# Kernel optimization log

Measured on AMD Instinct MI355X. Metric: run time of the kernel, lower is better.

Reference implementation:

```python
import jax, jax.numpy as jnp
import numpy as np

N = 50000      # nodes
E = 800000     # edges (avg degree 16)
EMB = 128      # emb_dim
NF = 7         # x_features
EF = 5         # edge_features
L = 5          # num_layer
BN_EPS = 1e-5


def setup_inputs() -> dict:
    key = jax.random.key(0)
    ks = jax.random.split(key, 12)
    s = 0.05
    return {
        "x": jax.random.normal(ks[0], (N, NF), jnp.float32),
        "edge_attr": jax.random.normal(ks[1], (E, EF), jnp.float32),
        "edge_index": jax.random.randint(ks[2], (2, E), 0, N, dtype=jnp.int32),
        "W_x": jax.random.normal(ks[3], (NF, EMB), jnp.float32) * s,
        "b_x": jax.random.normal(ks[4], (NF, EMB), jnp.float32) * s,
        "W_e": jax.random.normal(ks[5], (L, EF, EMB), jnp.float32) * s,
        "b_e": jax.random.normal(ks[6], (L, EF, EMB), jnp.float32) * s,
        # per-layer GIN update MLP: Linear(EMB,2EMB)-ReLU-Linear(2EMB,EMB)
        "W1": jax.random.normal(ks[7], (L, EMB, 2 * EMB), jnp.float32) * s,
        "b1": jnp.zeros((L, 2 * EMB), jnp.float32),
        "W2": jax.random.normal(ks[8], (L, 2 * EMB, EMB), jnp.float32) * s,
        "b2": jnp.zeros((L, EMB), jnp.float32),
        # per-layer BatchNorm1d affine params
        "gamma": jnp.ones((L, EMB), jnp.float32),
        "beta": jnp.zeros((L, EMB), jnp.float32),
    }


def reference(x, edge_attr, W_x, b_x, W_e, b_e, W1, b1, W2, b2, gamma, beta, edge_index):
    src, dst = edge_index[0], edge_index[1]
    # initial node embedding: sum of 7 Linear(1,EMB) applied per column == x @ W_x + sum(biases)
    h = x @ W_x + b_x.sum(axis=0)  # [N, EMB]
    for l in range(L):
        # edge embeddings: sum of EF Linear(1,EMB) over edge_attr columns
        e_emb = edge_attr @ W_e[l] + b_e[l].sum(axis=0)  # [E, EMB]
        sl_emb = b_e[l].sum(axis=0)  # self-loop edges have zero attr -> bias sum
        # message = x_j + edge_emb, aggr = add (scatter over dst); self loops add h + sl_emb
        msg = h[src] + e_emb                                        # [E, EMB]
        agg = jax.ops.segment_sum(msg, dst, num_segments=N) + h + sl_emb  # [N, EMB]
        # GIN update MLP
        z = jax.nn.relu(agg @ W1[l] + b1[l]) @ W2[l] + b2[l]        # [N, EMB]
        # BatchNorm1d (training-mode batch stats, biased variance)
        mu = z.mean(axis=0)
        var = z.var(axis=0)
        z = (z - mu) * jax.lax.rsqrt(var + BN_EPS) * gamma[l] + beta[l]
        # ELU on all but last layer; dropout is identity at drop_ratio=0; JK='last'
        h = jax.nn.elu(z) if l < L - 1 else z
    return h
```

## Files before the change

kernel.cpp:

```cpp
#include <hip/hip_runtime.h>
#include <math.h>

#define NN 50000
#define NE 800000
#define EMB 128
#define HID 256
#define NF 7
#define EF 5
#define NL 5
#define BN_EPS 1e-5f
#define NREP 32
#define SCAN_B 196

typedef _Float16 f16x8 __attribute__((ext_vector_type(8)));
typedef _Float16 f16x2 __attribute__((ext_vector_type(2)));
typedef __attribute__((ext_vector_type(4))) float f32x4;

__device__ inline unsigned pkh2(float a, float b) {
    union { unsigned v; _Float16 h[2]; } x;
    x.h[0] = (_Float16)a; x.h[1] = (_Float16)b;
    return x.v;
}
__device__ inline float2 uph2(unsigned u) {
    union { unsigned v; _Float16 h[2]; } x; x.v = u;
    return make_float2((float)x.h[0], (float)x.h[1]);
}
__device__ inline unsigned short f2h_bits(float f) {
    _Float16 h = (_Float16)f;
    return __builtin_bit_cast(unsigned short, h);
}
__device__ inline float h_bits2f(unsigned short b) {
    return (float)__builtin_bit_cast(_Float16, b);
}
__device__ inline f16x2 as_h2(unsigned u) { return __builtin_bit_cast(f16x2, u); }

__global__ void k_prep(const float* __restrict__ b_x, const float* __restrict__ b_e,
                       float* __restrict__ bsum_x, float* __restrict__ bsum_e,
                       int* __restrict__ counts, int* __restrict__ cursor) {
    int tid = threadIdx.x;
    if (blockIdx.x == 0 && tid < EMB) {
        float s = 0.f;
        for (int f = 0; f < NF; ++f) s += b_x[f * EMB + tid];
        bsum_x[tid] = s;
        for (int l = 0; l < NL; ++l) {
            float se = 0.f;
            for (int f = 0; f < EF; ++f) se += b_e[(l * EF + f) * EMB + tid];
            bsum_e[l * EMB + tid] = se;
        }
    }
    int gid = blockIdx.x * blockDim.x + tid;
    int stride = gridDim.x * blockDim.x;
    for (int i = gid; i < NN; i += stride) { counts[i] = 0; cursor[i] = 0; }
}

__global__ void k_prepw(const float* __restrict__ W1, const float* __restrict__ W2,
                        unsigned short* __restrict__ W1ph, unsigned short* __restrict__ W1pl,
                        unsigned short* __restrict__ W2ph, unsigned short* __restrict__ W2pl) {
    const int TOT = NL * EMB * HID;
    int gid = blockIdx.x * blockDim.x + threadIdx.x;
    if (gid < TOT) {
        int l = gid / (EMB * HID);
        int r = gid % (EMB * HID);
        int w = r >> 13;
        int rem = r & 8191;
        int h2 = rem >> 11;
        int rem2 = rem & 2047;
        int kk = rem2 >> 9;
        int rem3 = rem2 & 511;
        int lane = rem3 >> 3;
        int j = rem3 & 7;
        int hc = w * 64 + h2 * 16 + (lane & 15);
        int k = kk * 32 + (lane >> 4) * 8 + j;
        float wv = W1[((size_t)l * EMB + k) * HID + hc];
        unsigned short hi = f2h_bits(wv);
        W1ph[gid] = hi;
        W1pl[gid] = f2h_bits(wv - h_bits2f(hi));
    } else if (gid < 2 * TOT) {
        int g = gid - TOT;
        int l = g / (EMB * HID);
        int r = g % (EMB * HID);
        int w = r >> 13;
        int rem = r & 8191;
        int o2 = rem >> 12;
        int rem2 = rem & 4095;
        int kk = rem2 >> 9;
        int rem3 = rem2 & 511;
        int lane = rem3 >> 3;
        int j = rem3 & 7;
        int oc = w * 32 + o2 * 16 + (lane & 15);
        int k2 = kk * 32 + (lane >> 4) * 8 + j;
        float wv = W2[((size_t)l * HID + k2) * EMB + oc];
        unsigned short hi = f2h_bits(wv);
        W2ph[g] = hi;
        W2pl[g] = f2h_bits(wv - h_bits2f(hi));
    }
}

__global__ void k_init(const float* __restrict__ x, const float* __restrict__ W_x,
                       const float* __restrict__ bsum_x, unsigned short* __restrict__ h16) {
    int gid = blockIdx.x * blockDim.x + threadIdx.x;
    int v = gid >> 5;
    if (v >= NN) return;
    int c = (gid & 31) << 2;
    float4 acc = *(const float4*)(bsum_x + c);
    #pragma unroll
    for (int f = 0; f < NF; ++f) {
        float xv = x[(size_t)v * NF + f];
        float4 w = *(const float4*)(W_x + f * EMB + c);
        acc.x += xv * w.x; acc.y += xv * w.y; acc.z += xv * w.z; acc.w += xv * w.w;
    }
    uint2 p = make_uint2(pkh2(acc.x, acc.y), pkh2(acc.z, acc.w));
    *(uint2*)(h16 + (size_t)v * EMB + c) = p;
}

__global__ void k_hist(const int* __restrict__ dst, int* __restrict__ counts) {
    int e = blockIdx.x * blockDim.x + threadIdx.x;
    if (e < NE) atomicAdd(&counts[dst[e]], 1);
}

__global__ void k_scan1(const int* __restrict__ counts, int* __restrict__ bsum) {
    int tid = threadIdx.x;
    int i = blockIdx.x * 256 + tid;
    int v = (i < NN) ? counts[i] : 0;
    #pragma unroll
    for (int off = 1; off < 64; off <<= 1) v += __shfl_xor(v, off, 64);
    __shared__ int ws[4];
    if ((tid & 63) == 0) ws[tid >> 6] = v;
    __syncthreads();
    if (tid == 0) bsum[blockIdx.x] = ws[0] + ws[1] + ws[2] + ws[3];
}

__global__ void k_scan2(const int* __restrict__ bsum, int* __restrict__ bpre,
                        int* __restrict__ row_start) {
    int tid = threadIdx.x;
    int x = (tid < SCAN_B) ? bsum[tid] : 0;
    int lane = tid & 63, wv = tid >> 6;
    int v = x;
    #pragma unroll
    for (int off = 1; off < 64; off <<= 1) {
        int t = __shfl_up(v, off, 64);
        if (lane >= off) v += t;
    }
    __shared__ int wsum[4];
    if (lane == 63) wsum[wv] = v;
    __syncthreads();
    int woff = 0;
    #pragma unroll
    for (int w = 0; w < 4; ++w) if (w < wv) woff += wsum[w];
    int incl = v + woff;
    if (tid < SCAN_B) bpre[tid] = incl - x;
    if (tid == 255) row_start[NN] = incl;
}

__global__ void k_scan3(const int* __restrict__ counts, const int* __restrict__ bpre,
                        int* __restrict__ row_start) {
    int tid = threadIdx.x;
    int i = blockIdx.x * 256 + tid;
    int x = (i < NN) ? counts[i] : 0;
    int lane = tid & 63, wv = tid >> 6;
    int v = x;
    #pragma unroll
    for (int off = 1; off < 64; off <<= 1) {
        int t = __shfl_up(v, off, 64);
        if (lane >= off) v += t;
    }
    __shared__ int wsum[4];
    if (lane == 63) wsum[wv] = v;
    __syncthreads();
    int woff = 0;
    #pragma unroll
    for (int w = 0; w < 4; ++w) if (w < wv) woff += wsum[w];
    if (i < NN) row_start[i] = bpre[blockIdx.x] + v + woff - x;
}

__global__ void k_fill(const int* __restrict__ src, const int* __restrict__ dst,
                       const float* __restrict__ edge_attr,
                       const int* __restrict__ row_start, int* __restrict__ cursor,
                       uint4* __restrict__ sorted_pk) {
    int e = blockIdx.x * blockDim.x + threadIdx.x;
    if (e >= NE) return;
    int d = dst[e];
    int pos = atomicAdd(&cursor[d], 1);
    int idx = row_start[d] + pos;
    const float* ea = edge_attr + (size_t)e * EF;
    float a0 = ea[0], a1 = ea[1], a2 = ea[2], a3 = ea[3], a4 = ea[4];
    uint4 pk;
    pk.x = (unsigned)src[e];
    pk.y = pkh2(a0, a1);
    pk.z = pkh2(a2, a3);
    pk.w = pkh2(a4, 0.f);
    sorted_pk[idx] = pk;
}

__global__ void k_esum(const uint4* __restrict__ sorted_pk,
                       const int* __restrict__ row_start,
                       float* __restrict__ attsum, int* __restrict__ sorted_srcc) {
    int v = blockIdx.x * blockDim.x + threadIdx.x;
    if (v >= NN) return;
    int e0 = row_start[v], e1 = row_start[v + 1];
    float s0 = 0.f, s1 = 0.f, s2 = 0.f, s3 = 0.f, s4 = 0.f;
    for (int e = e0; e < e1; ++e) {
        uint4 pk = sorted_pk[e];
        sorted_srcc[e] = (int)pk.x;
        float2 a01 = uph2(pk.y), a23 = uph2(pk.z), a4x = uph2(pk.w);
        s0 += a01.x; s1 += a01.y; s2 += a23.x; s3 += a23.y; s4 += a4x.x;
    }
    float* o = attsum + (size_t)v * 8;
    *(float4*)(o) = make_float4(s0, s1, s2, s3);
    *(float4*)(o + 4) = make_float4(s4, (float)(e1 - e0), 0.f, 0.f);
}

__global__ __launch_bounds__(256) void k_agg(
        const unsigned short* __restrict__ h16, const int* __restrict__ sorted_srcc,
        const float* __restrict__ attsum,
        const float* __restrict__ W_e_l, const float* __restrict__ bsum_e_l,
        const int* __restrict__ row_start,
        unsigned short* __restrict__ agg16, float* __restrict__ stats) {
    int tid = threadIdx.x;
    if (blockIdx.x < NREP) stats[blockIdx.x * 2 * EMB + tid] = 0.f;
    int gid = blockIdx.x * 256 + tid;
    int v = gid >> 6;
    if (v >= NN) return;
    int c = (gid & 63) << 1;
    float2 we0 = *(const float2*)(W_e_l + 0 * EMB + c);
    float2 we1 = *(const float2*)(W_e_l + 1 * EMB + c);
    float2 we2 = *(const float2*)(W_e_l + 2 * EMB + c);
    float2 we3 = *(const float2*)(W_e_l + 3 * EMB + c);
    float2 we4 = *(const float2*)(W_e_l + 4 * EMB + c);
    float2 bs = *(const float2*)(bsum_e_l + c);
    float2 hv = uph2(*(const unsigned*)(h16 + (size_t)v * EMB + c));
    const float* at = attsum + (size_t)v * 8;
    float4 a03 = *(const float4*)(at);
    float2 a45 = *(const float2*)(at + 4);
    float ax = hv.x + (a45.y + 1.f) * bs.x
             + a03.x*we0.x + a03.y*we1.x + a03.z*we2.x + a03.w*we3.x + a45.x*we4.x;
    float ay = hv.y + (a45.y + 1.f) * bs.y
             + a03.x*we0.y + a03.y*we1.y + a03.z*we2.y + a03.w*we3.y + a45.x*we4.y;
    int e0 = row_start[v], e1 = row_start[v + 1];
    int e = e0;
    for (; e + 8 <= e1; e += 8) {
        int s0 = __builtin_amdgcn_readfirstlane(sorted_srcc[e + 0]);
        int s1 = __builtin_amdgcn_readfirstlane(sorted_srcc[e + 1]);
        int s2 = __builtin_amdgcn_readfirstlane(sorted_srcc[e + 2]);
        int s3 = __builtin_amdgcn_readfirstlane(sorted_srcc[e + 3]);
        int s4 = __builtin_amdgcn_readfirstlane(sorted_srcc[e + 4]);
        int s5 = __builtin_amdgcn_readfirstlane(sorted_srcc[e + 5]);
        int s6 = __builtin_amdgcn_readfirstlane(sorted_srcc[e + 6]);
        int s7 = __builtin_amdgcn_readfirstlane(sorted_srcc[e + 7]);
        unsigned u0 = *(const unsigned*)(h16 + (size_t)s0 * EMB + c);
        unsigned u1 = *(const unsigned*)(h16 + (size_t)s1 * EMB + c);
        unsigned u2 = *(const unsigned*)(h16 + (size_t)s2 * EMB + c);
        unsigned u3 = *(const unsigned*)(h16 + (size_t)s3 * EMB + c);
        unsigned u4 = *(const unsigned*)(h16 + (size_t)s4 * EMB + c);
        unsigned u5 = *(const unsigned*)(h16 + (size_t)s5 * EMB + c);
        unsigned u6 = *(const unsigned*)(h16 + (size_t)s6 * EMB + c);
        unsigned u7 = *(const unsigned*)(h16 + (size_t)s7 * EMB + c);
        f16x2 p01 = as_h2(u0) + as_h2(u1);
        f16x2 p23 = as_h2(u2) + as_h2(u3);
        f16x2 p45 = as_h2(u4) + as_h2(u5);
        f16x2 p67 = as_h2(u6) + as_h2(u7);
        f16x2 p03 = p01 + p23;
        f16x2 p47 = p45 + p67;
        f16x2 p07 = p03 + p47;
        ax += (float)p07.x;
        ay += (float)p07.y;
    }
    for (; e < e1; ++e) {
        int s = __builtin_amdgcn_readfirstlane(sorted_srcc[e]);
        float2 hs = uph2(*(const unsigned*)(h16 + (size_t)s * EMB + c));
        ax += hs.x;
        ay += hs.y;
    }
    *(unsigned*)(agg16 + (size_t)v * EMB + c) = pkh2(ax, ay);
}

__global__ __launch_bounds__(256) void k_mlp(
        const unsigned short* __restrict__ agg16,
        const unsigned short* __restrict__ W1ph, const unsigned short* __restrict__ W1pl,
        const float* __restrict__ b1_l,
        const unsigned short* __restrict__ W2ph, const unsigned short* __restrict__ W2pl,
        const float* __restrict__ b2_l,
        unsigned short* __restrict__ z16, float* __restrict__ stats) {
    __shared__ unsigned short A16[32][136];
    __shared__ unsigned short Hid16[32][264];
    int tid = threadIdx.x;
    int r0 = blockIdx.x * 32;
    int rep = blockIdx.x & (NREP - 1);
    #pragma unroll
    for (int it = 0; it < 2; ++it) {
        int idx = it * 256 + tid;
        int row = idx >> 4;
        int cb = (idx & 15) * 8;
        int grow = r0 + row;
        uint4 val = make_uint4(0u, 0u, 0u, 0u);
        if (grow < NN) val = *(const uint4*)(agg16 + (size_t)grow * EMB + cb);
        *(uint4*)(&A16[row][cb]) = val;
    }
    __syncthreads();
    int wave = tid >> 6, lane = tid & 63;
    int l16 = lane & 15, quad = lane >> 4;
    {
        f16x8 af[2][4];
        #pragma unroll
        for (int nt = 0; nt < 2; ++nt)
            #pragma unroll
            for (int kk = 0; kk < 4; ++kk)
                af[nt][kk] = *(const f16x8*)(&A16[nt * 16 + l16][kk * 32 + quad * 8]);
        #pragma unroll
        for (int h2 = 0; h2 < 4; ++h2) {
            f16x8 whf[4], wlf[4];
            #pragma unroll
            for (int kk = 0; kk < 4; ++kk) {
                size_t off = ((((size_t)(wave * 4 + h2) * 4) + kk) * 64 + lane) * 8;
                whf[kk] = *(const f16x8*)(W1ph + off);
                wlf[kk] = *(const f16x8*)(W1pl + off);
            }
            float4 bv = *(const float4*)(b1_l + wave * 64 + h2 * 16 + quad * 4);
            f32x4 bias = {bv.x, bv.y, bv.z, bv.w};
            #pragma unroll
            for (int nt = 0; nt < 2; ++nt) {
                f32x4 acc = bias;
                #pragma unroll
                for (int kk = 0; kk < 4; ++kk)
                    acc = __builtin_amdgcn_mfma_f32_16x16x32_f16(whf[kk], af[nt][kk], acc, 0, 0, 0);
                #pragma unroll
                for (int kk = 0; kk < 4; ++kk)
                    acc = __builtin_amdgcn_mfma_f32_16x16x32_f16(wlf[kk], af[nt][kk], acc, 0, 0, 0);
                uint2 p;
                p.x = pkh2(fmaxf(acc[0], 0.f), fmaxf(acc[1], 0.f));
                p.y = pkh2(fmaxf(acc[2], 0.f), fmaxf(acc[3], 0.f));
                int col = wave * 64 + h2 * 16 + quad * 4;
                *(uint2*)(&Hid16[nt * 16 + l16][col]) = p;
            }
        }
    }
    __syncthreads();
    float ss[2][4] = {}, sq[2][4] = {};
    #pragma unroll
    for (int o2 = 0; o2 < 2; ++o2) {
        f16x8 w2h[8], w2l[8];
        #pragma unroll
        for (int kk = 0; kk < 8; ++kk) {
            size_t off = ((((size_t)(wave * 2 + o2) * 8) + kk) * 64 + lane) * 8;
            w2h[kk] = *(const f16x8*)(W2ph + off);
            w2l[kk] = *(const f16x8*)(W2pl + off);
        }
        float4 bv = *(const float4*)(b2_l + wave * 32 + o2 * 16 + quad * 4);
        f32x4 bias = {bv.x, bv.y, bv.z, bv.w};
        #pragma unroll
        for (int nt = 0; nt < 2; ++nt) {
            f16x8 hf[8];
            #pragma unroll
            for (int kk = 0; kk < 8; ++kk)
                hf[kk] = *(const f16x8*)(&Hid16[nt * 16 + l16][kk * 32 + quad * 8]);
            f32x4 acc = bias;
            #pragma unroll
            for (int kk = 0; kk < 8; ++kk)
                acc = __builtin_amdgcn_mfma_f32_16x16x32_f16(w2h[kk], hf[kk], acc, 0, 0, 0);
            #pragma unroll
            for (int kk = 0; kk < 8; ++kk)
                acc = __builtin_amdgcn_mfma_f32_16x16x32_f16(w2l[kk], hf[kk], acc, 0, 0, 0);
            int node = r0 + nt * 16 + l16;
            if (node < NN) {
                uint2 p = make_uint2(pkh2(acc[0], acc[1]), pkh2(acc[2], acc[3]));
                *(uint2*)(z16 + (size_t)node * EMB + wave * 32 + o2 * 16 + quad * 4) = p;
                #pragma unroll
                for (int r = 0; r < 4; ++r) {
                    ss[o2][r] += acc[r];
                    sq[o2][r] += acc[r] * acc[r];
                }
            }
        }
    }
    #pragma unroll
    for (int o2 = 0; o2 < 2; ++o2)
        #pragma unroll
        for (int r = 0; r < 4; ++r) {
            float s = ss[o2][r], q = sq[o2][r];
            #pragma unroll
            for (int m = 1; m < 16; m <<= 1) {
                s += __shfl_xor(s, m, 64);
                q += __shfl_xor(q, m, 64);
            }
            if (l16 == 0) {
                int oc = wave * 32 + o2 * 16 + quad * 4 + r;
                atomicAdd(&stats[rep * 2 * EMB + oc], s);
                atomicAdd(&stats[rep * 2 * EMB + EMB + oc], q);
            }
        }
}

__global__ void k_bnscale(const float* __restrict__ stats,
                          const float* __restrict__ gamma_l, const float* __restrict__ beta_l,
                          float* __restrict__ scsh) {
    int tid = threadIdx.x;
    float s = 0.f, q = 0.f;
    #pragma unroll
    for (int r = 0; r < NREP; ++r) {
        s += stats[r * 2 * EMB + tid];
        q += stats[r * 2 * EMB + EMB + tid];
    }
    float mu = s * (1.f / NN);
    float var = q * (1.f / NN) - mu * mu;
    float sf = gamma_l[tid] * rsqrtf(var + BN_EPS);
    scsh[tid] = sf;
    scsh[EMB + tid] = beta_l[tid] - mu * sf;
}

__global__ void k_bn(const unsigned short* __restrict__ z16, const float* __restrict__ scsh,
                     unsigned short* __restrict__ h16, float* __restrict__ fout, int last) {
    __shared__ float sc[EMB], sh[EMB];
    int tid = threadIdx.x;
    if (tid < EMB) {
        sc[tid] = scsh[tid];
        sh[tid] = scsh[EMB + tid];
    }
    __syncthreads();
    int gid = blockIdx.x * blockDim.x + tid;
    if (gid >= NN * EMB / 4) return;
    int c = (gid & 31) << 2;
    uint2 zp = *(const uint2*)(z16 + (size_t)gid * 4);
    float2 z01 = uph2(zp.x), z23 = uph2(zp.y);
    float o0 = z01.x * sc[c + 0] + sh[c + 0];
    float o1 = z01.y * sc[c + 1] + sh[c + 1];
    float o2 = z23.x * sc[c + 2] + sh[c + 2];
    float o3 = z23.y * sc[c + 3] + sh[c + 3];
    if (!last) {
        o0 = (o0 > 0.f) ? o0 : (__expf(o0) - 1.f);
        o1 = (o1 > 0.f) ? o1 : (__expf(o1) - 1.f);
        o2 = (o2 > 0.f) ? o2 : (__expf(o2) - 1.f);
        o3 = (o3 > 0.f) ? o3 : (__expf(o3) - 1.f);
        uint2 p = make_uint2(pkh2(o0, o1), pkh2(o2, o3));
        *(uint2*)(h16 + (size_t)gid * 4) = p;
    } else {
        *(float4*)(fout + (size_t)gid * 4) = make_float4(o0, o1, o2, o3);
    }
}

extern "C" void kernel_launch(void* const* d_in, const int* in_sizes, int n_in,
                              void* d_out, int out_size, void* d_ws, size_t ws_size,
                              hipStream_t stream) {
    const float* x         = (const float*)d_in[0];
    const float* edge_attr = (const float*)d_in[1];
    const int*   edge_idx  = (const int*)d_in[2];
    const float* W_x   = (const float*)d_in[3];
    const float* b_x   = (const float*)d_in[4];
    const float* W_e   = (const float*)d_in[5];
    const float* b_e   = (const float*)d_in[6];
    const float* W1    = (const float*)d_in[7];
    const float* b1    = (const float*)d_in[8];
    const float* W2    = (const float*)d_in[9];
    const float* b2    = (const float*)d_in[10];
    const float* gamma = (const float*)d_in[11];
    const float* beta  = (const float*)d_in[12];
    float* fout = (float*)d_out;

    const int* src = edge_idx;
    const int* dst = edge_idx + NE;

    char* p = (char*)d_ws;
    auto alloc = [&](size_t bytes) { char* q = p; p += (bytes + 255) & ~(size_t)255; return q; };
    unsigned short* h16  = (unsigned short*)alloc((size_t)NN * EMB * 2);
    unsigned short* z16  = (unsigned short*)alloc((size_t)NN * EMB * 2);
    unsigned short* agg16 = (unsigned short*)alloc((size_t)NN * EMB * 2);
    unsigned short* W1ph = (unsigned short*)alloc((size_t)NL * HID * EMB * 2);
    unsigned short* W1pl = (unsigned short*)alloc((size_t)NL * HID * EMB * 2);
    unsigned short* W2ph = (unsigned short*)alloc((size_t)NL * EMB * HID * 2);
    unsigned short* W2pl = (unsigned short*)alloc((size_t)NL * EMB * HID * 2);
    int*   row_start  = (int*)alloc((NN + 1) * sizeof(int));
    int*   counts     = (int*)alloc(NN * sizeof(int));
    int*   cursor     = (int*)alloc(NN * sizeof(int));
    uint4* sorted_pk  = (uint4*)alloc((size_t)NE * sizeof(uint4));
    int*   sorted_srcc= (int*)alloc((size_t)NE * sizeof(int));
    float* attsum     = (float*)alloc((size_t)NN * 8 * sizeof(float));
    int*   bsum       = (int*)alloc(SCAN_B * sizeof(int));
    int*   bpre       = (int*)alloc(SCAN_B * sizeof(int));
    float* stats      = (float*)alloc((size_t)NREP * 2 * EMB * sizeof(float));
    float* scsh       = (float*)alloc(2 * EMB * sizeof(float));
    float* bsum_x     = (float*)alloc(EMB * sizeof(float));
    float* bsum_e     = (float*)alloc(NL * EMB * sizeof(float));

    k_prep<<<256, 256, 0, stream>>>(b_x, b_e, bsum_x, bsum_e, counts, cursor);
    k_prepw<<<(2 * NL * EMB * HID + 255) / 256, 256, 0, stream>>>(W1, W2, W1ph, W1pl, W2ph, W2pl);
    k_init<<<(NN * 32 + 255) / 256, 256, 0, stream>>>(x, W_x, bsum_x, h16);
    k_hist<<<(NE + 255) / 256, 256, 0, stream>>>(dst, counts);
    k_scan1<<<SCAN_B, 256, 0, stream>>>(counts, bsum);
    k_scan2<<<1, 256, 0, stream>>>(bsum, bpre, row_start);
    k_scan3<<<SCAN_B, 256, 0, stream>>>(counts, bpre, row_start);
    k_fill<<<(NE + 255) / 256, 256, 0, stream>>>(src, dst, edge_attr, row_start, cursor,
                                                 sorted_pk);
    k_esum<<<SCAN_B, 256, 0, stream>>>(sorted_pk, row_start, attsum, sorted_srcc);
    const int AGG_GRID = (NN * 64 + 255) / 256;
    for (int l = 0; l < NL; ++l) {
        k_agg<<<AGG_GRID, 256, 0, stream>>>(
            h16, sorted_srcc, attsum,
            W_e + (size_t)l * EF * EMB, bsum_e + l * EMB, row_start,
            agg16, stats);
        k_mlp<<<(NN + 31) / 32, 256, 0, stream>>>(
            agg16,
            W1ph + (size_t)l * HID * EMB, W1pl + (size_t)l * HID * EMB, b1 + (size_t)l * HID,
            W2ph + (size_t)l * EMB * HID, W2pl + (size_t)l * EMB * HID, b2 + (size_t)l * EMB,
            z16, stats);
        k_bnscale<<<1, 128, 0, stream>>>(stats, gamma + l * EMB, beta + l * EMB, scsh);
        k_bn<<<(NN * EMB / 4 + 255) / 256, 256, 0, stream>>>(
            z16, scsh, h16, fout, (l == NL - 1) ? 1 : 0);
    }
}
```

Measured before the change: 613.6 us.

## Two-pass bucketed edge scatter for CSR build and 64-row MLP tiles

Replaces the single random-scatter CSR fill with a two-pass sort. Edges are first grouped into 1024-node destination buckets using shared-memory counters and one global atomic per bucket per block. A second pass then places them into final CSR order from the more local grouped array, improving write locality and atomic contention. Separately, the MLP kernel now processes 64 rows per block instead of 32, amortizing weight fragment loads over more rows at the cost of more LDS and registers. The dst index is packed into the upper 16 bits of the last word, which only holds for node ids below 65536.

Result: faster. 581.1 us (-5.3%).

```diff
diff --git a/kernel.cpp b/kernel.cpp
--- a/kernel.cpp
+++ b/kernel.cpp
@@ -11,6 +11,7 @@
 #define BN_EPS 1e-5f
 #define NREP 32
 #define SCAN_B 196
+#define NBUCK 49
 
 typedef _Float16 f16x8 __attribute__((ext_vector_type(8)));
 typedef _Float16 f16x2 __attribute__((ext_vector_type(2)));
@@ -153,7 +154,7 @@
 }
 
 __global__ void k_scan3(const int* __restrict__ counts, const int* __restrict__ bpre,
-                        int* __restrict__ row_start) {
+                        int* __restrict__ row_start, int* __restrict__ bcur) {
     int tid = threadIdx.x;
     int i = blockIdx.x * 256 + tid;
     int x = (i < NN) ? counts[i] : 0;
@@ -170,26 +171,68 @@
     int woff = 0;
     #pragma unroll
     for (int w = 0; w < 4; ++w) if (w < wv) woff += wsum[w];
-    if (i < NN) row_start[i] = bpre[blockIdx.x] + v + woff - x;
-}
-
-__global__ void k_fill(const int* __restrict__ src, const int* __restrict__ dst,
-                       const float* __restrict__ edge_attr,
-                       const int* __restrict__ row_start, int* __restrict__ cursor,
-                       uint4* __restrict__ sorted_pk) {
+    if (i < NN) {
+        int rs = bpre[blockIdx.x] + v + woff - x;
+        row_start[i] = rs;
+        if ((i & 1023) == 0) bcur[i >> 10] = rs;
+    }
+}
+
+#define BPB 2048
+__global__ __launch_bounds__(256) void k_bucket(
+        const int* __restrict__ src, const int* __restrict__ dst,
+        const float* __restrict__ edge_attr,
+        int* __restrict__ bcur, uint4* __restrict__ grouped) {
+    __shared__ int lcnt[NBUCK];
+    __shared__ int lbase[NBUCK];
+    int tid = threadIdx.x;
+    if (tid < NBUCK) lcnt[tid] = 0;
+    __syncthreads();
+    int base = blockIdx.x * BPB;
+    int b_[8];
+    int d_[8];
+    #pragma unroll
+    for (int k = 0; k < 8; ++k) {
+        int e = base + k * 256 + tid;
+        if (e < NE) {
+            int d = dst[e];
+            d_[k] = d;
+            b_[k] = d >> 10;
+            atomicAdd(&lcnt[b_[k]], 1);
+        } else b_[k] = -1;
+    }
+    __syncthreads();
+    if (tid < NBUCK) {
+        lbase[tid] = (lcnt[tid] > 0) ? atomicAdd(&bcur[tid], lcnt[tid]) : 0;
+        lcnt[tid] = 0;
+    }
+    __syncthreads();
+    #pragma unroll
+    for (int k = 0; k < 8; ++k) {
+        int e = base + k * 256 + tid;
+        if (e < NE) {
+            int b = b_[k];
+            int off = lbase[b] + atomicAdd(&lcnt[b], 1);
+            const float* ea = edge_attr + (size_t)e * EF;
+            uint4 pk;
+            pk.x = (unsigned)src[e];
+            pk.y = pkh2(ea[0], ea[1]);
+            pk.z = pkh2(ea[2], ea[3]);
+            pk.w = (unsigned)f2h_bits(ea[4]) | ((unsigned)d_[k] << 16);
+            grouped[off] = pk;
+        }
+    }
+}
+
+__global__ void k_place(const uint4* __restrict__ grouped,
+                        const int* __restrict__ row_start, int* __restrict__ cursor,
+                        uint4* __restrict__ sorted_pk) {
     int e = blockIdx.x * blockDim.x + threadIdx.x;
     if (e >= NE) return;
-    int d = dst[e];
+    uint4 pk = grouped[e];
+    int d = (int)(pk.w >> 16);
     int pos = atomicAdd(&cursor[d], 1);
-    int idx = row_start[d] + pos;
-    const float* ea = edge_attr + (size_t)e * EF;
-    float a0 = ea[0], a1 = ea[1], a2 = ea[2], a3 = ea[3], a4 = ea[4];
-    uint4 pk;
-    pk.x = (unsigned)src[e];
-    pk.y = pkh2(a0, a1);
-    pk.z = pkh2(a2, a3);
-    pk.w = pkh2(a4, 0.f);
-    sorted_pk[idx] = pk;
+    sorted_pk[row_start[d] + pos] = pk;
 }
 
 __global__ void k_esum(const uint4* __restrict__ sorted_pk,
@@ -202,8 +245,9 @@
     for (int e = e0; e < e1; ++e) {
         uint4 pk = sorted_pk[e];
         sorted_srcc[e] = (int)pk.x;
-        float2 a01 = uph2(pk.y), a23 = uph2(pk.z), a4x = uph2(pk.w);
-        s0 += a01.x; s1 += a01.y; s2 += a23.x; s3 += a23.y; s4 += a4x.x;
+        float2 a01 = uph2(pk.y), a23 = uph2(pk.z);
+        s0 += a01.x; s1 += a01.y; s2 += a23.x; s3 += a23.y;
+        s4 += h_bits2f((unsigned short)(pk.w & 0xffffu));
     }
     float* o = attsum + (size_t)v * 8;
     *(float4*)(o) = make_float4(s0, s1, s2, s3);
@@ -281,13 +325,13 @@
         const unsigned short* __restrict__ W2ph, const unsigned short* __restrict__ W2pl,
         const float* __restrict__ b2_l,
         unsigned short* __restrict__ z16, float* __restrict__ stats) {
-    __shared__ unsigned short A16[32][136];
-    __shared__ unsigned short Hid16[32][264];
-    int tid = threadIdx.x;
-    int r0 = blockIdx.x * 32;
+    __shared__ unsigned short A16[64][136];
+    __shared__ unsigned short Hid16[64][264];
+    int tid = threadIdx.x;
+    int r0 = blockIdx.x * 64;
     int rep = blockIdx.x & (NREP - 1);
     #pragma unroll
-    for (int it = 0; it < 2; ++it) {
+    for (int it = 0; it < 4; ++it) {
         int idx = it * 256 + tid;
         int row = idx >> 4;
         int cb = (idx & 15) * 8;
@@ -300,9 +344,9 @@
     int wave = tid >> 6, lane = tid & 63;
     int l16 = lane & 15, quad = lane >> 4;
     {
-        f16x8 af[2][4];
+        f16x8 af[4][4];
         #pragma unroll
-        for (int nt = 0; nt < 2; ++nt)
+        for (int nt = 0; nt < 4; ++nt)
             #pragma unroll
             for (int kk = 0; kk < 4; ++kk)
                 af[nt][kk] = *(const f16x8*)(&A16[nt * 16 + l16][kk * 32 + quad * 8]);
@@ -318,7 +362,7 @@
             float4 bv = *(const float4*)(b1_l + wave * 64 + h2 * 16 + quad * 4);
             f32x4 bias = {bv.x, bv.y, bv.z, bv.w};
             #pragma unroll
-            for (int nt = 0; nt < 2; ++nt) {
+            for (int nt = 0; nt < 4; ++nt) {
                 f32x4 acc = bias;
                 #pragma unroll
                 for (int kk = 0; kk < 4; ++kk)
@@ -348,7 +392,7 @@
         float4 bv = *(const float4*)(b2_l + wave * 32 + o2 * 16 + quad * 4);
         f32x4 bias = {bv.x, bv.y, bv.z, bv.w};
         #pragma unroll
-        for (int nt = 0; nt < 2; ++nt) {
+        for (int nt = 0; nt < 4; ++nt) {
             f16x8 hf[8];
             #pragma unroll
             for (int kk = 0; kk < 8; ++kk)
@@ -470,11 +514,13 @@
     int*   row_start  = (int*)alloc((NN + 1) * sizeof(int));
     int*   counts     = (int*)alloc(NN * sizeof(int));
     int*   cursor     = (int*)alloc(NN * sizeof(int));
+    uint4* grouped    = (uint4*)alloc((size_t)NE * sizeof(uint4));
     uint4* sorted_pk  = (uint4*)alloc((size_t)NE * sizeof(uint4));
     int*   sorted_srcc= (int*)alloc((size_t)NE * sizeof(int));
     float* attsum     = (float*)alloc((size_t)NN * 8 * sizeof(float));
     int*   bsum       = (int*)alloc(SCAN_B * sizeof(int));
     int*   bpre       = (int*)alloc(SCAN_B * sizeof(int));
+    int*   bcur       = (int*)alloc(NBUCK * sizeof(int));
     float* stats      = (float*)alloc((size_t)NREP * 2 * EMB * sizeof(float));
     float* scsh       = (float*)alloc(2 * EMB * sizeof(float));
     float* bsum_x     = (float*)alloc(EMB * sizeof(float));
@@ -486,9 +532,9 @@
     k_hist<<<(NE + 255) / 256, 256, 0, stream>>>(dst, counts);
     k_scan1<<<SCAN_B, 256, 0, stream>>>(counts, bsum);
     k_scan2<<<1, 256, 0, stream>>>(bsum, bpre, row_start);
-    k_scan3<<<SCAN_B, 256, 0, stream>>>(counts, bpre, row_start);
-    k_fill<<<(NE + 255) / 256, 256, 0, stream>>>(src, dst, edge_attr, row_start, cursor,
-                                                 sorted_pk);
+    k_scan3<<<SCAN_B, 256, 0, stream>>>(counts, bpre, row_start, bcur);
+    k_bucket<<<(NE + BPB - 1) / BPB, 256, 0, stream>>>(src, dst, edge_attr, bcur, grouped);
+    k_place<<<(NE + 255) / 256, 256, 0, stream>>>(grouped, row_start, cursor, sorted_pk);
     k_esum<<<SCAN_B, 256, 0, stream>>>(sorted_pk, row_start, attsum, sorted_srcc);
     const int AGG_GRID = (NN * 64 + 255) / 256;
     for (int l = 0; l < NL; ++l) {
@@ -496,7 +542,7 @@
             h16, sorted_srcc, attsum,
             W_e + (size_t)l * EF * EMB, bsum_e + l * EMB, row_start,
             agg16, stats);
-        k_mlp<<<(NN + 31) / 32, 256, 0, stream>>>(
+        k_mlp<<<(NN + 63) / 64, 256, 0, stream>>>(
             agg16,
             W1ph + (size_t)l * HID * EMB, W1pl + (size_t)l * HID * EMB, b1 + (size_t)l * HID,
             W2ph + (size_t)l * EMB * HID, W2pl + (size_t)l * EMB * HID, b2 + (size_t)l * EMB,
```
